# Kernel optimization log

Measured on AMD Instinct MI355X. Metric: run time of the kernel, lower is better.

The kernel has to match this reference:

```python
import jax, jax.numpy as jnp
import numpy as np

B, H, W, C = 32, 112, 112, 192
KH = KW = 3


def setup_inputs() -> dict:
    key = jax.random.key(0)
    k1, k2 = jax.random.split(key)
    x = jax.random.normal(k1, (B, H, W, C), dtype=jnp.float32)
    # depthwise kernel, HWIO with I=1 and feature_group_count=C (depth_multiplier=1)
    w = jax.random.normal(k2, (KH, KW, 1, C), dtype=jnp.float32) * 0.1
    b = jnp.zeros((C,), dtype=jnp.float32)
    return {"x": x, "w": w, "b": b}


def reference(x, w, b):
    # Depthwise conv = grouped conv with feature_group_count == channels_in.
    # stride 1, 'same' padding, dilation 1, depth_multiplier 1, linear activation.
    out = jax.lax.conv_general_dilated(
        x, w,
        window_strides=(1, 1),
        padding='SAME',
        rhs_dilation=(1, 1),
        dimension_numbers=('NHWC', 'HWIO', 'NHWC'),
        feature_group_count=C,
    )
    return out + b  # bias broadcast over channel axis
```

## Files before the change

### kernel.cpp

```cpp
#include <hip/hip_runtime.h>


constexpr int Bn = 32, Hn = 112, Wn = 112, Cn = 192, C4 = 48;
constexpr int HT = 4, WT = 16, CT = 16;
constexpr int NSTEP = 7;
constexpr int HG = 4;
constexpr int WTiles = 7, CTiles = 3;
constexpr int LW = 20;
constexpr int ROWF4 = LW * CT;
constexpr int ROWB = ROWF4 * 16;
constexpr int RING = 10;

typedef float floatx4 __attribute__((ext_vector_type(4)));

__device__ __forceinline__ floatx4 fma4(floatx4 a, floatx4 b, floatx4 c) {
  c.x = fmaf(a.x, b.x, c.x);
  c.y = fmaf(a.y, b.y, c.y);
  c.z = fmaf(a.z, b.z, c.z);
  c.w = fmaf(a.w, b.w, c.w);
  return c;
}

__global__ __launch_bounds__(256, 3) void dwconv3x3_stream(
    const float* __restrict__ x,
    const float* __restrict__ wgt,
    const float* __restrict__ bias,
    float* __restrict__ out) {
  __shared__ floatx4 lds[RING * ROWF4];
  const int tid = (int)threadIdx.x;
  const int lane = tid & 63;
  const int wave = tid >> 6;

  int bid = blockIdx.x;
  int chunk = gridDim.x >> 3;
  int sbid = (bid & 7) * chunk + (bid >> 3);
  int c4t = sbid % CTiles; int t0 = sbid / CTiles;
  int wt = t0 % WTiles;    t0 /= WTiles;
  int hg = t0 % HG;        int b = t0 / HG;

  const int hbase = hg * (HT * NSTEP);
  const int w0 = wt * WT;
  const int cbase = c4t * (CT * 4);
  const float* xb = x + (long)b * Hn * Wn * Cn;

  int colOff[5];
  {
    int c4l = lane & 15;
#pragma unroll
    for (int j = 0; j < 5; ++j) {
      int wi = j * 4 + (lane >> 4);
      int wg = w0 + wi - 1;
      int wc = min(max(wg, 0), Wn - 1);
      colOff[j] = wc * Cn + cbase + c4l * 4;
    }
  }

  auto stageRow = [&](int row) {
    int h = hbase + row - 1;
    int hc = min(max(h, 0), Hn - 1);
    const float* rowp = xb + (long)hc * (Wn * Cn);
    int slot = row % RING;
    char* ldsbase = (char*)lds + slot * ROWB;
#pragma unroll
    for (int j = 0; j < 5; ++j) {
      __builtin_amdgcn_global_load_lds(
          (const __attribute__((address_space(1))) void*)(rowp + colOff[j]),
          (__attribute__((address_space(3))) void*)(ldsbase + j * 1024),
          16, 0, 0);
    }
  };

  stageRow(wave);
  stageRow(4 + (wave & 1));

  const int c4i = tid & 15;
  const int wi1 = tid >> 4;
  const int cofs = cbase + c4i * 4;
  const int wg1 = w0 + wi1;
  const float cs0 = (wg1 >= 1) ? 1.f : 0.f;
  const float cs2 = (wg1 <= Wn - 2) ? 1.f : 0.f;
  floatx4 wv[3][3];
#pragma unroll
  for (int kh = 0; kh < 3; ++kh) {
#pragma unroll
    for (int kw = 0; kw < 3; ++kw)
      wv[kh][kw] = *(const floatx4*)(wgt + (kh * 3 + kw) * Cn + cofs);
    wv[kh][0] *= cs0;
    wv[kh][2] *= cs2;
  }
  const floatx4 bv = *(const floatx4*)(bias + cofs);

  const float sTop = (hg == 0) ? 0.f : 1.f;
  const float sBot = (hg == HG - 1) ? 0.f : 1.f;

  const int ostrideF4 = Wn * C4;
  floatx4* outp = (floatx4*)out +
      ((long)b * Hn + hbase) * ostrideF4 + (long)wg1 * C4 + c4t * CT + c4i;

#pragma unroll
  for (int t = 0; t < NSTEP; ++t) {
    stageRow(4 * t + 6 + wave);
    if (t == 0) asm volatile("s_waitcnt vmcnt(5)" ::: "memory");
    else        asm volatile("s_waitcnt vmcnt(9)" ::: "memory");
    __builtin_amdgcn_s_barrier();

    floatx4 acc[HT];
#pragma unroll
    for (int o = 0; o < HT; ++o) acc[o] = bv;

#pragma unroll
    for (int r = 0; r < 6; ++r) {
      const int slot = (4 * t + r) % RING;
      const floatx4* base = lds + slot * ROWF4 + wi1 * 16 + c4i;
      floatx4 xv0 = base[0];
      floatx4 xv1 = base[16];
      floatx4 xv2 = base[32];
      if (t == 0 && r == 0) { xv0 *= sTop; xv1 *= sTop; xv2 *= sTop; }
      if (t == NSTEP - 1 && r == 5) { xv0 *= sBot; xv1 *= sBot; xv2 *= sBot; }
#pragma unroll
      for (int kh = 0; kh < 3; ++kh) {
        int o = r - kh;
        if (o >= 0 && o < HT) {
          acc[o] = fma4(xv0, wv[kh][0], acc[o]);
          acc[o] = fma4(xv1, wv[kh][1], acc[o]);
          acc[o] = fma4(xv2, wv[kh][2], acc[o]);
        }
      }
    }

#pragma unroll
    for (int o = 0; o < HT; ++o)
      __builtin_nontemporal_store(acc[o], outp + (long)(4 * t + o) * ostrideF4);

    __builtin_amdgcn_s_barrier();
  }
}

extern "C" void kernel_launch(void* const* d_in, const int* in_sizes, int n_in,
                              void* d_out, int out_size, void* d_ws, size_t ws_size,
                              hipStream_t stream) {
  const float* x = (const float*)d_in[0];
  const float* w = (const float*)d_in[1];
  const float* b = (const float*)d_in[2];
  float* out = (float*)d_out;

  const int grid = Bn * HG * WTiles * CTiles;
  dwconv3x3_stream<<<grid, 256, 0, stream>>>(x, w, b, out);
}
```

Measured before the change: 106.9 us.

## Trim LDS halo width and restructure row ring into 3-slot region buffer

Result: slower. 114.7 us (+7.2%).

```diff
diff --git a/kernel.cpp b/kernel.cpp
--- a/kernel.cpp
+++ b/kernel.cpp
@@ -2,14 +2,14 @@
 
 
 constexpr int Bn = 32, Hn = 112, Wn = 112, Cn = 192, C4 = 48;
-constexpr int HT = 4, WT = 16, CT = 16;
-constexpr int NSTEP = 7;
-constexpr int HG = 4;
+constexpr int WT = 16, CT = 16;
 constexpr int WTiles = 7, CTiles = 3;
-constexpr int LW = 20;
-constexpr int ROWF4 = LW * CT;
-constexpr int ROWB = ROWF4 * 16;
-constexpr int RING = 10;
+constexpr int NSTEP = 14, HG = 2;
+constexpr int LWC = 18;
+constexpr int ROWF4 = LWC * CT;
+constexpr int REGF4 = 4 * ROWF4;
+constexpr int REGB = REGF4 * 16;
+constexpr int NSLOT = 3;
 
 typedef float floatx4 __attribute__((ext_vector_type(4)));
 
@@ -21,57 +21,65 @@
   return c;
 }
 
-__global__ __launch_bounds__(256, 3) void dwconv3x3_stream(
+__global__ __launch_bounds__(256, 2) void dwconv3x3_stream2(
     const float* __restrict__ x,
     const float* __restrict__ wgt,
     const float* __restrict__ bias,
     float* __restrict__ out) {
-  __shared__ floatx4 lds[RING * ROWF4];
+  __shared__ floatx4 lds[NSLOT * REGF4];
   const int tid = (int)threadIdx.x;
   const int lane = tid & 63;
   const int wave = tid >> 6;
 
   int bid = blockIdx.x;
-  int chunk = gridDim.x >> 3;
-  int sbid = (bid & 7) * chunk + (bid >> 3);
-  int c4t = sbid % CTiles; int t0 = sbid / CTiles;
-  int wt = t0 % WTiles;    t0 /= WTiles;
-  int hg = t0 % HG;        int b = t0 / HG;
+  int chk = gridDim.x >> 3;
+  int sbid = (bid & 7) * chk + (bid >> 3);
+  int c4t = sbid % CTiles; int tt = sbid / CTiles;
+  int wt = tt % WTiles;    tt /= WTiles;
+  int hg = tt % HG;        int b = tt / HG;
 
-  const int hbase = hg * (HT * NSTEP);
+  const int hbase = hg * (4 * NSTEP);
   const int w0 = wt * WT;
   const int cbase = c4t * (CT * 4);
   const float* xb = x + (long)b * Hn * Wn * Cn;
+  const int rstr = Wn * Cn;
 
+  const int cstart = (wave < 2) ? wave * 5 : 10 + (wave - 2) * 4;
+  const int ccount = (wave < 2) ? 5 : 4;
+  int rr[5];
   int colOff[5];
-  {
-    int c4l = lane & 15;
 #pragma unroll
-    for (int j = 0; j < 5; ++j) {
-      int wi = j * 4 + (lane >> 4);
-      int wg = w0 + wi - 1;
-      int wc = min(max(wg, 0), Wn - 1);
-      colOff[j] = wc * Cn + cbase + c4l * 4;
-    }
+  for (int j = 0; j < 5; ++j) {
+    int c = cstart + j;
+    int l = c * 64 + lane;
+    int r = l / ROWF4;
+    int rem = l - r * ROWF4;
+    int wi = rem >> 4, c4l = rem & 15;
+    int wg = w0 + wi - 1;
+    int wc = min(max(wg, 0), Wn - 1);
+    rr[j] = r;
+    colOff[j] = wc * Cn + cbase + c4l * 4;
   }
 
-  auto stageRow = [&](int row) {
+  for (int c = wave; c < 27; c += 4) {
+    bool pre = c < 9;
+    int cc = pre ? c : c - 9;
+    int l = cc * 64 + lane;
+    int r = l / ROWF4;
+    int rem = l - r * ROWF4;
+    int wi = rem >> 4, c4l = rem & 15;
+    int row = pre ? r : 2 + r;
     int h = hbase + row - 1;
     int hc = min(max(h, 0), Hn - 1);
-    const float* rowp = xb + (long)hc * (Wn * Cn);
-    int slot = row % RING;
-    char* ldsbase = (char*)lds + slot * ROWB;
-#pragma unroll
-    for (int j = 0; j < 5; ++j) {
-      __builtin_amdgcn_global_load_lds(
-          (const __attribute__((address_space(1))) void*)(rowp + colOff[j]),
-          (__attribute__((address_space(3))) void*)(ldsbase + j * 1024),
-          16, 0, 0);
-    }
-  };
-
-  stageRow(wave);
-  stageRow(4 + (wave & 1));
+    int wg = w0 + wi - 1;
+    int wc = min(max(wg, 0), Wn - 1);
+    const float* src = xb + (long)hc * rstr + wc * Cn + cbase + c4l * 4;
+    char* dst = (char*)lds +
+        (pre ? (2 * REGB + 2 * ROWF4 * 16 + cc * 1024) : (cc * 1024));
+    __builtin_amdgcn_global_load_lds(
+        (const __attribute__((address_space(1))) void*)src,
+        (__attribute__((address_space(3))) void*)dst, 16, 0, 0);
+  }
 
   const int c4i = tid & 15;
   const int wi1 = tid >> 4;
@@ -89,38 +97,61 @@
     wv[kh][2] *= cs2;
   }
   const floatx4 bv = *(const floatx4*)(bias + cofs);
-
   const float sTop = (hg == 0) ? 0.f : 1.f;
   const float sBot = (hg == HG - 1) ? 0.f : 1.f;
 
-  const int ostrideF4 = Wn * C4;
+  const int ostr = Wn * C4;
   floatx4* outp = (floatx4*)out +
-      ((long)b * Hn + hbase) * ostrideF4 + (long)wg1 * C4 + c4t * CT + c4i;
+      ((long)b * Hn + hbase) * ostr + (long)wg1 * C4 + c4t * CT + c4i;
+  const int ldaddr = wi1 * CT + c4i;
 
 #pragma unroll
   for (int t = 0; t < NSTEP; ++t) {
-    stageRow(4 * t + 6 + wave);
-    if (t == 0) asm volatile("s_waitcnt vmcnt(5)" ::: "memory");
-    else        asm volatile("s_waitcnt vmcnt(9)" ::: "memory");
+    if (t < NSTEP - 1) {
+      char* rbase = (char*)lds + ((t + 1) % 3) * REGB;
+      const int R0 = 4 * (t + 1) + 2;
+#pragma unroll
+      for (int j = 0; j < 5; ++j) {
+        if (j < ccount) {
+          int h = hbase + R0 + rr[j] - 1;
+          int hc = min(h, Hn - 1);
+          const float* src = xb + (long)hc * rstr + colOff[j];
+          __builtin_amdgcn_global_load_lds(
+              (const __attribute__((address_space(1))) void*)src,
+              (__attribute__((address_space(3))) void*)(rbase + (cstart + j) * 1024),
+              16, 0, 0);
+        }
+      }
+    }
+    if (t == 0) {
+      if (wave < 2) asm volatile("s_waitcnt vmcnt(5)" ::: "memory");
+      else          asm volatile("s_waitcnt vmcnt(4)" ::: "memory");
+    } else if (t < NSTEP - 1) {
+      if (wave < 2) asm volatile("s_waitcnt vmcnt(9)" ::: "memory");
+      else          asm volatile("s_waitcnt vmcnt(8)" ::: "memory");
+    } else {
+      asm volatile("s_waitcnt vmcnt(4)" ::: "memory");
+    }
     __builtin_amdgcn_s_barrier();
 
-    floatx4 acc[HT];
+    floatx4 acc[4];
 #pragma unroll
-    for (int o = 0; o < HT; ++o) acc[o] = bv;
+    for (int o = 0; o < 4; ++o) acc[o] = bv;
 
 #pragma unroll
     for (int r = 0; r < 6; ++r) {
-      const int slot = (4 * t + r) % RING;
-      const floatx4* base = lds + slot * ROWF4 + wi1 * 16 + c4i;
+      const int slot = (r < 2) ? (t + 2) % 3 : t % 3;
+      const int rowoff = (r < 2) ? r + 2 : r - 2;
+      const floatx4* base = lds + slot * REGF4 + rowoff * ROWF4 + ldaddr;
       floatx4 xv0 = base[0];
-      floatx4 xv1 = base[16];
-      floatx4 xv2 = base[32];
+      floatx4 xv1 = base[CT];
+      floatx4 xv2 = base[2 * CT];
       if (t == 0 && r == 0) { xv0 *= sTop; xv1 *= sTop; xv2 *= sTop; }
       if (t == NSTEP - 1 && r == 5) { xv0 *= sBot; xv1 *= sBot; xv2 *= sBot; }
 #pragma unroll
       for (int kh = 0; kh < 3; ++kh) {
         int o = r - kh;
-        if (o >= 0 && o < HT) {
+        if (o >= 0 && o < 4) {
           acc[o] = fma4(xv0, wv[kh][0], acc[o]);
           acc[o] = fma4(xv1, wv[kh][1], acc[o]);
           acc[o] = fma4(xv2, wv[kh][2], acc[o]);
@@ -129,8 +160,8 @@
     }
 
 #pragma unroll
-    for (int o = 0; o < HT; ++o)
-      __builtin_nontemporal_store(acc[o], outp + (long)(4 * t + o) * ostrideF4);
+    for (int o = 0; o < 4; ++o)
+      __builtin_nontemporal_store(acc[o], outp + (long)(4 * t + o) * ostr);
 
     __builtin_amdgcn_s_barrier();
   }
@@ -145,5 +176,5 @@
   float* out = (float*)d_out;
 
   const int grid = Bn * HG * WTiles * CTiles;
-  dwconv3x3_stream<<<grid, 256, 0, stream>>>(x, w, b, out);
+  dwconv3x3_stream2<<<grid, 256, 0, stream>>>(x, w, b, out);
 }
```

## Give each wave a private LDS ring and drop block barriers

Applied to the files above, without the earlier changes.

Result: no change. 107.8 us (+0.8%).

```diff
diff --git a/kernel.cpp b/kernel.cpp
--- a/kernel.cpp
+++ b/kernel.cpp
@@ -2,16 +2,16 @@
 
 
 constexpr int Bn = 32, Hn = 112, Wn = 112, Cn = 192, C4 = 48;
-constexpr int HT = 4, WT = 16, CT = 16;
+constexpr int PW = 8, PC = 8;
+constexpr int WP = 14, CP = 6, HG = 4;
 constexpr int NSTEP = 7;
-constexpr int HG = 4;
-constexpr int WTiles = 7, CTiles = 3;
-constexpr int LW = 20;
-constexpr int ROWF4 = LW * CT;
-constexpr int ROWB = ROWF4 * 16;
-constexpr int RING = 10;
+constexpr int ROWB = 10 * PC * 16;
+constexpr int GRPB = 5 * 1024;
+constexpr int WLDS = 3 * GRPB;
 
 typedef float floatx4 __attribute__((ext_vector_type(4)));
+
+#define VMWAIT(n) asm volatile("s_waitcnt vmcnt(" #n ")" ::: "memory")
 
 __device__ __forceinline__ floatx4 fma4(floatx4 a, floatx4 b, floatx4 c) {
   c.x = fmaf(a.x, b.x, c.x);
@@ -21,64 +21,62 @@
   return c;
 }
 
-__global__ __launch_bounds__(256, 3) void dwconv3x3_stream(
+__global__ __launch_bounds__(128, 2) void dwconv3x3_wavepriv(
     const float* __restrict__ x,
     const float* __restrict__ wgt,
     const float* __restrict__ bias,
     float* __restrict__ out) {
-  __shared__ floatx4 lds[RING * ROWF4];
+  __shared__ char lds[2 * WLDS];
   const int tid = (int)threadIdx.x;
   const int lane = tid & 63;
   const int wave = tid >> 6;
 
   int bid = blockIdx.x;
-  int chunk = gridDim.x >> 3;
-  int sbid = (bid & 7) * chunk + (bid >> 3);
-  int c4t = sbid % CTiles; int t0 = sbid / CTiles;
-  int wt = t0 % WTiles;    t0 /= WTiles;
-  int hg = t0 % HG;        int b = t0 / HG;
+  int chk = gridDim.x >> 3;
+  int sbid = (bid & 7) * chk + (bid >> 3);
+  int pid = sbid * 2 + wave;
+  int cp = pid % CP;  int t1 = pid / CP;
+  int wp = t1 % WP;   t1 /= WP;
+  int hg = t1 & 3;    int b = t1 >> 2;
 
-  const int hbase = hg * (HT * NSTEP);
-  const int w0 = wt * WT;
-  const int cbase = c4t * (CT * 4);
+  const int hbase = hg * 28;
+  const int w0 = wp * PW;
   const float* xb = x + (long)b * Hn * Wn * Cn;
+  const int rstr = Wn * Cn;
+  char* wl = lds + wave * WLDS;
 
-  int colOff[5];
-  {
-    int c4l = lane & 15;
+  int rowadd[5], coloff[5];
 #pragma unroll
-    for (int j = 0; j < 5; ++j) {
-      int wi = j * 4 + (lane >> 4);
-      int wg = w0 + wi - 1;
-      int wc = min(max(wg, 0), Wn - 1);
-      colOff[j] = wc * Cn + cbase + c4l * 4;
-    }
+  for (int k = 0; k < 5; ++k) {
+    int q = k * 64 + lane;
+    rowadd[k] = q / 80;
+    int rem = q % 80;
+    int col = rem >> 3, c4 = rem & 7;
+    int wc = min(max(w0 + col - 1, 0), Wn - 1);
+    coloff[k] = wc * Cn + cp * 32 + c4 * 4;
   }
 
-  auto stageRow = [&](int row) {
-    int h = hbase + row - 1;
-    int hc = min(max(h, 0), Hn - 1);
-    const float* rowp = xb + (long)hc * (Wn * Cn);
-    int slot = row % RING;
-    char* ldsbase = (char*)lds + slot * ROWB;
+  auto stage = [&](int g) {
+    char* dst0 = wl + (g % 3) * GRPB;
 #pragma unroll
-    for (int j = 0; j < 5; ++j) {
+    for (int k = 0; k < 5; ++k) {
+      int h = min(max(hbase + 4 * g + rowadd[k] - 1, 0), Hn - 1);
+      const float* src = xb + (long)h * rstr + coloff[k];
       __builtin_amdgcn_global_load_lds(
-          (const __attribute__((address_space(1))) void*)(rowp + colOff[j]),
-          (__attribute__((address_space(3))) void*)(ldsbase + j * 1024),
+          (const __attribute__((address_space(1))) void*)src,
+          (__attribute__((address_space(3))) void*)(dst0 + k * 1024),
           16, 0, 0);
     }
   };
 
-  stageRow(wave);
-  stageRow(4 + (wave & 1));
+  stage(0); stage(1); stage(2);
 
-  const int c4i = tid & 15;
-  const int wi1 = tid >> 4;
-  const int cofs = cbase + c4i * 4;
-  const int wg1 = w0 + wi1;
-  const float cs0 = (wg1 >= 1) ? 1.f : 0.f;
-  const float cs2 = (wg1 <= Wn - 2) ? 1.f : 0.f;
+  const int c4i = lane & 7;
+  const int wi = lane >> 3;
+  const int cofs = cp * 32 + c4i * 4;
+  const int wg = w0 + wi;
+  const float cs0 = (wg >= 1) ? 1.f : 0.f;
+  const float cs2 = (wg <= Wn - 2) ? 1.f : 0.f;
   floatx4 wv[3][3];
 #pragma unroll
   for (int kh = 0; kh < 3; ++kh) {
@@ -89,38 +87,38 @@
     wv[kh][2] *= cs2;
   }
   const floatx4 bv = *(const floatx4*)(bias + cofs);
-
   const float sTop = (hg == 0) ? 0.f : 1.f;
   const float sBot = (hg == HG - 1) ? 0.f : 1.f;
 
-  const int ostrideF4 = Wn * C4;
+  const int ostr = Wn * C4;
   floatx4* outp = (floatx4*)out +
-      ((long)b * Hn + hbase) * ostrideF4 + (long)wg1 * C4 + c4t * CT + c4i;
+      ((long)(b * Hn + hbase) * Wn + wg) * C4 + cp * PC + c4i;
 
 #pragma unroll
   for (int t = 0; t < NSTEP; ++t) {
-    stageRow(4 * t + 6 + wave);
-    if (t == 0) asm volatile("s_waitcnt vmcnt(5)" ::: "memory");
-    else        asm volatile("s_waitcnt vmcnt(9)" ::: "memory");
-    __builtin_amdgcn_s_barrier();
+    if (t == 0)      VMWAIT(5);
+    else if (t == 1) VMWAIT(9);
+    else if (t < 6)  VMWAIT(13);
+    else             VMWAIT(8);
 
-    floatx4 acc[HT];
+    floatx4 acc[4];
 #pragma unroll
-    for (int o = 0; o < HT; ++o) acc[o] = bv;
+    for (int o = 0; o < 4; ++o) acc[o] = bv;
 
 #pragma unroll
     for (int r = 0; r < 6; ++r) {
-      const int slot = (4 * t + r) % RING;
-      const floatx4* base = lds + slot * ROWF4 + wi1 * 16 + c4i;
-      floatx4 xv0 = base[0];
-      floatx4 xv1 = base[16];
-      floatx4 xv2 = base[32];
+      const int s = 4 * t + r;
+      const char* base =
+          wl + (s >> 2) % 3 * GRPB + (s & 3) * ROWB + 128 + lane * 16;
+      floatx4 xv0 = *(const floatx4*)(base - 128);
+      floatx4 xv1 = *(const floatx4*)(base);
+      floatx4 xv2 = *(const floatx4*)(base + 128);
       if (t == 0 && r == 0) { xv0 *= sTop; xv1 *= sTop; xv2 *= sTop; }
       if (t == NSTEP - 1 && r == 5) { xv0 *= sBot; xv1 *= sBot; xv2 *= sBot; }
 #pragma unroll
       for (int kh = 0; kh < 3; ++kh) {
         int o = r - kh;
-        if (o >= 0 && o < HT) {
+        if (o >= 0 && o < 4) {
           acc[o] = fma4(xv0, wv[kh][0], acc[o]);
           acc[o] = fma4(xv1, wv[kh][1], acc[o]);
           acc[o] = fma4(xv2, wv[kh][2], acc[o]);
@@ -128,11 +126,13 @@
       }
     }
 
+    asm volatile("s_waitcnt lgkmcnt(0)" ::: "memory");
+    __builtin_amdgcn_sched_barrier(0);
+    if (t <= 4) stage(t + 3);
+
 #pragma unroll
-    for (int o = 0; o < HT; ++o)
-      __builtin_nontemporal_store(acc[o], outp + (long)(4 * t + o) * ostrideF4);
-
-    __builtin_amdgcn_s_barrier();
+    for (int o = 0; o < 4; ++o)
+      __builtin_nontemporal_store(acc[o], outp + (long)(4 * t + o) * ostr);
   }
 }
 
@@ -144,6 +144,6 @@
   const float* b = (const float*)d_in[2];
   float* out = (float*)d_out;
 
-  const int grid = Bn * HG * WTiles * CTiles;
-  dwconv3x3_stream<<<grid, 256, 0, stream>>>(x, w, b, out);
+  const int grid = Bn * HG * WP * CP / 2;
+  dwconv3x3_wavepriv<<<grid, 128, 0, stream>>>(x, w, b, out);
 }
```
